# Kernel tuning notes

Hardware: AMD Instinct MI355X
Metric: run time of the kernel (lower is better)

Reference implementation:

```python
import jax, jax.numpy as jnp
import numpy as np

H = 4096
GROUP = 128          # per-token activation quant group, also weight block size
EPS = 1e-6
FP8_MAX = 448.0      # float8_e4m3fn max


def fp8_roundtrip(v):
    # simulate fp8 storage: cast to e4m3 and back to f32
    return v.astype(jnp.float8_e4m3fn).astype(jnp.float32)


def rms_norm(x, w):
    # vLLM RMSNorm: x * rsqrt(mean(x^2) + eps) * weight, computed in f32
    var = jnp.mean(x * x, axis=-1, keepdims=True)
    return x * jax.lax.rsqrt(var + EPS) * w


def fused_add_rms_norm(x, resid, w):
    z = x + resid
    return rms_norm(z, w), z


def group_quant_dequant(y):
    # dynamic per-token-group (1,128) symmetric fp8 quant, then dequant
    T, Hd = y.shape
    yg = y.reshape(T, Hd // GROUP, GROUP)
    amax = jnp.max(jnp.abs(yg), axis=-1, keepdims=True)
    scale = jnp.maximum(amax, 1e-12) / FP8_MAX
    q = fp8_roundtrip(yg / scale)
    return (q * scale).reshape(T, Hd)


def block_fp8_linear(y, wq, wscale):
    # W8A8 block fp8 GEMM: act quant (1,128) groups, weight (128,128) block scales.
    # Math-equivalent form: dequantize both operands, then GEMM.
    a = group_quant_dequant(y)                                   # [T, H]
    ws = jnp.repeat(jnp.repeat(wscale, GROUP, 0), GROUP, 1)       # [H, H]
    w = wq * ws                                                   # dequant weight
    return a @ w                                                  # [T, H]


def setup_inputs() -> dict:
    key = jax.random.key(0)
    ks = jax.random.split(key, 8)
    T = 16384
    x = jax.random.normal(ks[0], (T, H), dtype=jnp.float32)
    norm_w = jnp.ones((4, H), dtype=jnp.float32)
    # weights: rand in [0,1) stored as fp8 (simulated by roundtrip)
    w0 = fp8_roundtrip(jax.random.uniform(ks[1], (H, H), dtype=jnp.float32))
    w1 = fp8_roundtrip(jax.random.uniform(ks[2], (H, H), dtype=jnp.float32))
    w2 = fp8_roundtrip(jax.random.uniform(ks[3], (H, H), dtype=jnp.float32))
    sh = H // GROUP
    ws0 = jax.random.uniform(ks[4], (sh, sh), dtype=jnp.float32)
    ws1 = jax.random.uniform(ks[5], (sh, sh), dtype=jnp.float32)
    ws2 = jax.random.uniform(ks[6], (sh, sh), dtype=jnp.float32)
    return {"x": x, "norm_w": norm_w, "w0": w0, "w1": w1, "w2": w2,
            "ws0": ws0, "ws1": ws1, "ws2": ws2}


def reference(x, norm_w, w0, w1, w2, ws0, ws1, ws2):
    x = jax.nn.relu(x)
    resid = x
    y = rms_norm(x, norm_w[0])
    x2 = block_fp8_linear(y, w0, ws0)
    y2, resid = fused_add_rms_norm(x2, resid, norm_w[1])
    x3 = block_fp8_linear(y2, w1, ws1)
    y3, resid = fused_add_rms_norm(x3, resid, norm_w[2])
    x4 = block_fp8_linear(y3, w2, ws2)
    y4, resid = fused_add_rms_norm(x4, resid, norm_w[3])
    return y4
```

## Files before the change

kernel.cpp:

```cpp
#include <hip/hip_runtime.h>

typedef __attribute__((ext_vector_type(4))) float f32x4;
typedef __attribute__((ext_vector_type(4))) unsigned int u32x4;
typedef __attribute__((ext_vector_type(4))) int i32x4;
typedef __attribute__((ext_vector_type(8))) int i32x8;
typedef __attribute__((ext_vector_type(4))) unsigned short u16x4;
typedef unsigned char u8;
typedef unsigned short u16;
typedef unsigned int u32;

#define MBYTE (1024*1024)
#define TTOK 16384
#define HDIM 4096

__device__ __forceinline__ float f16tof32(u16 h) {
  _Float16 x;
  __builtin_memcpy(&x, &h, 2);
  return (float)x;
}
__device__ __forceinline__ u16 f32tof16(float f) {
  _Float16 x = (_Float16)f;
  u16 h;
  __builtin_memcpy(&h, &x, 2);
  return h;
}


__device__ __forceinline__ void gload_lds16(const void* g, void* l) {
  __builtin_amdgcn_global_load_lds((const __attribute__((address_space(1))) void*)g,
                                   (__attribute__((address_space(3))) void*)l, 16, 0, 0);
}

__global__ __launch_bounds__(256) void k_wconv(const float* __restrict__ w0,
                                               const float* __restrict__ w1,
                                               const float* __restrict__ w2,
                                               u8* __restrict__ out) {
  __shared__ float tl[64][68];
  const int tid = threadIdx.x;
  const int bn = blockIdx.x, bk = blockIdx.y, z = blockIdx.z;
  const float* W = (z == 0) ? w0 : (z == 1 ? w1 : w2);
  u8* o = out + (size_t)z * 16 * MBYTE;
#pragma unroll
  for (int it = 0; it < 4; ++it) {
    int idx = it * 256 + tid;
    int r = idx >> 4, c4 = idx & 15;
    f32x4 v = *(const f32x4*)(W + (size_t)(bk * 64 + r) * HDIM + bn * 64 + c4 * 4);
    *(f32x4*)&tl[r][c4 * 4] = v;
  }
  __syncthreads();
  {
    int n = tid >> 2, q4 = tid & 3;
    u32 dw[4];
#pragma unroll
    for (int d = 0; d < 4; ++d) {
      int k0 = (d >> 1) * 32 + q4 * 8 + (d & 1) * 4;
      int w = __builtin_amdgcn_cvt_pk_fp8_f32(tl[k0 + 0][n], tl[k0 + 1][n], 0, false);
      w = __builtin_amdgcn_cvt_pk_fp8_f32(tl[k0 + 2][n], tl[k0 + 3][n], w, true);
      dw[d] = (u32)w;
    }
    u32x4 pack = {dw[0], dw[1], dw[2], dw[3]};
    *(u32x4*)(o + (size_t)(bn * 64 + n) * HDIM + (bk >> 1) * 128 + (bk & 1) * 64 + q4 * 16) = pack;
  }
}

template <int MODE>
__global__ __launch_bounds__(256) void k_norm(const void* __restrict__ in_,
                                              u16* __restrict__ resid,
                                              const float* __restrict__ nw,
                                              u32* __restrict__ qout,
                                              float* __restrict__ asct,
                                              float* __restrict__ yout) {
  const int row = blockIdx.x, t = threadIdx.x;
  u16x4* residr = (u16x4*)(resid + (size_t)row * HDIM);
  f32x4 v[4];
  float ss = 0.f;
#pragma unroll
  for (int j = 0; j < 4; ++j) {
    f32x4 a;
    if (MODE == 1) {
      const u16x4* inr = (const u16x4*)((const u16*)in_ + (size_t)row * HDIM);
      u16x4 iv = inr[j * 256 + t];
      a.x = f16tof32(iv.x); a.y = f16tof32(iv.y);
      a.z = f16tof32(iv.z); a.w = f16tof32(iv.w);
    } else {
      const f32x4* inr = (const f32x4*)((const float*)in_ + (size_t)row * HDIM);
      a = inr[j * 256 + t];
    }
    if (MODE == 0) {
      a.x = fmaxf(a.x, 0.f); a.y = fmaxf(a.y, 0.f);
      a.z = fmaxf(a.z, 0.f); a.w = fmaxf(a.w, 0.f);
    } else {
      u16x4 rz = residr[j * 256 + t];
      a.x += f16tof32(rz.x); a.y += f16tof32(rz.y);
      a.z += f16tof32(rz.z); a.w += f16tof32(rz.w);
    }
    if (MODE < 2) {
      u16x4 rw;
      rw.x = f32tof16(a.x); rw.y = f32tof16(a.y);
      rw.z = f32tof16(a.z); rw.w = f32tof16(a.w);
      residr[j * 256 + t] = rw;
    }
    v[j] = a;
    ss += a.x * a.x + a.y * a.y + a.z * a.z + a.w * a.w;
  }
#pragma unroll
  for (int m = 1; m <= 32; m <<= 1) ss += __shfl_xor(ss, m, 64);
  __shared__ float sred[4];
  if ((t & 63) == 0) sred[t >> 6] = ss;
  __syncthreads();
  float tot = sred[0] + sred[1] + sred[2] + sred[3];
  float rinv = rsqrtf(tot * (1.f / (float)HDIM) + 1e-6f);
#pragma unroll
  for (int j = 0; j < 4; ++j) {
    f32x4 nv = ((const f32x4*)nw)[j * 256 + t];
    f32x4 y;
    y.x = v[j].x * rinv * nv.x; y.y = v[j].y * rinv * nv.y;
    y.z = v[j].z * rinv * nv.z; y.w = v[j].w * rinv * nv.w;
    if (MODE == 2) {
      ((f32x4*)yout)[(size_t)row * 1024 + j * 256 + t] = y;
    } else {
      float am = fmaxf(fmaxf(fabsf(y.x), fabsf(y.y)), fmaxf(fabsf(y.z), fabsf(y.w)));
#pragma unroll
      for (int m = 1; m <= 16; m <<= 1) am = fmaxf(am, __shfl_xor(am, m, 64));
      am = fmaxf(am, 1e-12f);
      float scale = am / 448.f;
      float inv = 448.f / am;
      int d = __builtin_amdgcn_cvt_pk_fp8_f32(y.x * inv, y.y * inv, 0, false);
      d = __builtin_amdgcn_cvt_pk_fp8_f32(y.z * inv, y.w * inv, d, true);
      int k4 = j * 256 + t;
      int k4w = k4 & 31;
      int k4n = (k4 & ~31) | (((k4w >> 4) & 1) << 4) | (((k4w >> 1) & 3) << 2)
              | (((k4w >> 3) & 1) << 1) | (k4w & 1);
      qout[(size_t)row * 1024 + k4n] = (u32)d;
      if ((t & 31) == 0) asct[(size_t)(j * 8 + (t >> 5)) * TTOK + row] = scale;
    }
  }
}

template <int F16OUT>
__global__ __launch_bounds__(256, 2) void k_gemm(const u8* __restrict__ A,
                                                 const u8* __restrict__ B,
                                                 const float* __restrict__ aS,
                                                 const float* __restrict__ bS,
                                                 void* __restrict__ C) {
  __shared__ u8 Al[2][128 * 128];
  __shared__ u8 Bl[2][128 * 128];
  __shared__ float As[32 * 128];
  const int tid = threadIdx.x;
  const int lane = tid & 63, wave = tid >> 6;
  const int lin = blockIdx.x;
  const int xcd = lin & 7, tt = lin >> 3;
  const int sidx = tt >> 3, rr = tt & 7;
  const int sm = sidx >> 3, sn = sidx & 7;
  const int bm = xcd * 16 + sm * 2 + (rr >> 2);
  const int bn = sn * 4 + (rr & 3);
  const int brow = bm * 128, bcol = bn * 128;
  const int wrb = (wave >> 1) * 64, wcb = (wave & 1) * 64;
  const int r16 = lane & 15, q4 = lane >> 4;
  const int swz3 = r16 & 7;
  const int c0 = (q4 ^ swz3) << 4;
  const int c1 = ((4 + q4) ^ swz3) << 4;

  const int srow = tid >> 3;
  const int scol = (((tid & 7) ^ (srow & 7)) << 4);
  const u8* aP = A + (size_t)(brow + srow) * HDIM + scol;
  const u8* bP = B + (size_t)(bcol + srow) * HDIM + scol;
  const int ldst = tid * 16;

#define STAGE(c, kt) do {                                                       \
    _Pragma("unroll")                                                           \
    for (int i = 0; i < 4; ++i) {                                               \
      gload_lds16(aP + (size_t)(kt) * 128 + (size_t)i * 32 * HDIM,              \
                  &Al[c][i * 4096 + ldst]);                                     \
      gload_lds16(bP + (size_t)(kt) * 128 + (size_t)i * 32 * HDIM,              \
                  &Bl[c][i * 4096 + ldst]);                                     \
    }                                                                           \
  } while (0)

  f32x4 av[4];
#pragma unroll
  for (int i = 0; i < 4; ++i) {
    const int kt_ = i * 8 + (tid >> 5);
    const int r_ = (tid & 31) * 4;
    av[i] = *(const f32x4*)(aS + (size_t)kt_ * TTOK + brow + r_);
  }
  STAGE(0, 0);
  STAGE(1, 1);
  asm volatile("s_waitcnt vmcnt(16)" ::: "memory");
#pragma unroll
  for (int i = 0; i < 4; ++i)
    *(f32x4*)&As[i * 1024 + tid * 4] = av[i];
  asm volatile("s_waitcnt lgkmcnt(0)" ::: "memory");

  f32x4 accm[4][4] = {};
  const f32x4 z4 = {0.f, 0.f, 0.f, 0.f};

#pragma unroll 1
  for (int kt = 0; kt < 32; ++kt) {
    const int cur = kt & 1;
    if (kt < 31) asm volatile("s_waitcnt vmcnt(8)" ::: "memory");
    else         asm volatile("s_waitcnt vmcnt(0)" ::: "memory");
    __builtin_amdgcn_s_barrier();
    __builtin_amdgcn_sched_barrier(0);

    const float wsb = bS[kt * 32 + bn];

    i32x8 bfr[4];
#pragma unroll
    for (int n = 0; n < 4; ++n) {
      const u8* rp = &Bl[cur][(wcb + n * 16 + r16) * 128];
      i32x4 lo = *(const i32x4*)(rp + c0);
      i32x4 hi = *(const i32x4*)(rp + c1);
      bfr[n] = __builtin_shufflevector(lo, hi, 0, 1, 2, 3, 4, 5, 6, 7);
    }

#pragma unroll
    for (int m = 0; m < 4; ++m) {
      const u8* rp = &Al[cur][(wrb + m * 16 + r16) * 128];
      i32x4 lo = *(const i32x4*)(rp + c0);
      i32x4 hi = *(const i32x4*)(rp + c1);
      i32x8 afr = __builtin_shufflevector(lo, hi, 0, 1, 2, 3, 4, 5, 6, 7);
      const f32x4 sa = *(const f32x4*)&As[kt * 128 + wrb + m * 16 + q4 * 4];
      const f32x4 s = sa * wsb;
      f32x4 acc[4];
      __builtin_amdgcn_s_setprio(1);
#pragma unroll
      for (int n = 0; n < 4; ++n)
        acc[n] = __builtin_amdgcn_mfma_scale_f32_16x16x128_f8f6f4(
            afr, bfr[n], z4, 0, 0, 0, 0x7F7F7F7F, 0, 0x7F7F7F7F);
      __builtin_amdgcn_s_setprio(0);
#pragma unroll
      for (int n = 0; n < 4; ++n)
        accm[m][n] += acc[n] * s;
    }

    __builtin_amdgcn_sched_barrier(0);
    __builtin_amdgcn_s_barrier();
    if (kt < 30) STAGE(cur, kt + 2);
  }
#undef STAGE

#pragma unroll
  for (int m = 0; m < 4; ++m) {
#pragma unroll
    for (int r = 0; r < 4; ++r) {
      const size_t rowi = (size_t)(brow + wrb + m * 16 + q4 * 4 + r);
      if (F16OUT) {
        u16* Cp = (u16*)C + rowi * HDIM + bcol + wcb + r16;
#pragma unroll
        for (int n = 0; n < 4; ++n) Cp[n * 16] = f32tof16(accm[m][n][r]);
      } else {
        float* Cp = (float*)C + rowi * HDIM + bcol + wcb + r16;
#pragma unroll
        for (int n = 0; n < 4; ++n) Cp[n * 16] = accm[m][n][r];
      }
    }
  }
}

extern "C" void kernel_launch(void* const* d_in, const int* in_sizes, int n_in,
                              void* d_out, int out_size, void* d_ws, size_t ws_size,
                              hipStream_t stream) {
  const float* x  = (const float*)d_in[0];
  const float* nw = (const float*)d_in[1];
  const float* w0 = (const float*)d_in[2];
  const float* w1 = (const float*)d_in[3];
  const float* w2 = (const float*)d_in[4];
  const float* s0 = (const float*)d_in[5];
  const float* s1 = (const float*)d_in[6];
  const float* s2 = (const float*)d_in[7];
  float* out = (float*)d_out;
  char* ws = (char*)d_ws;

  u8*  wqt   = (u8*)ws;
  u32* q     = (u32*)(ws + (size_t)48 * MBYTE);
  float* asc = (float*)(ws + (size_t)112 * MBYTE);
  u16* rsd   = (u16*)(ws + (size_t)114 * MBYTE);

  k_wconv<<<dim3(64, 64, 3), 256, 0, stream>>>(w0, w1, w2, wqt);

  k_norm<0><<<TTOK, 256, 0, stream>>>(x, rsd, nw, q, asc, nullptr);
  k_gemm<1><<<4096, 256, 0, stream>>>((const u8*)q, wqt, asc, s0, d_out);

  k_norm<1><<<TTOK, 256, 0, stream>>>(d_out, rsd, nw + HDIM, q, asc, nullptr);
  k_gemm<1><<<4096, 256, 0, stream>>>((const u8*)q, wqt + (size_t)16 * MBYTE, asc, s1, d_out);

  k_norm<1><<<TTOK, 256, 0, stream>>>(d_out, rsd, nw + 2 * HDIM, q, asc, nullptr);
  k_gemm<0><<<4096, 256, 0, stream>>>((const u8*)q, wqt + (size_t)32 * MBYTE, asc, s2, d_out);

  k_norm<2><<<TTOK, 256, 0, stream>>>(d_out, rsd, nw + 3 * HDIM, nullptr, nullptr, out);
}
```

Before: 1.387 ms.

## Fuse residual add into GEMM epilogue and ping-pong fp16 residual buffers

The residual addition moves from the norm kernel into the GEMM epilogue. The GEMM now reads the fp16 residual, adds it to the accumulator and writes the sum z as fp16. The norm kernels then only read z, with no separate residual read and write, and two ping-pong workspace buffers hold z between stages. The last GEMM also writes fp16 instead of f32, which cuts traffic but adds an extra rounding step before the final norm.

```diff
diff --git a/kernel.cpp b/kernel.cpp
--- a/kernel.cpp
+++ b/kernel.cpp
@@ -65,40 +65,31 @@
 
 template <int MODE>
 __global__ __launch_bounds__(256) void k_norm(const void* __restrict__ in_,
-                                              u16* __restrict__ resid,
+                                              u16* __restrict__ zout,
                                               const float* __restrict__ nw,
                                               u32* __restrict__ qout,
                                               float* __restrict__ asct,
                                               float* __restrict__ yout) {
   const int row = blockIdx.x, t = threadIdx.x;
-  u16x4* residr = (u16x4*)(resid + (size_t)row * HDIM);
   f32x4 v[4];
   float ss = 0.f;
 #pragma unroll
   for (int j = 0; j < 4; ++j) {
     f32x4 a;
-    if (MODE == 1) {
+    if (MODE == 0) {
+      const f32x4* inr = (const f32x4*)((const float*)in_ + (size_t)row * HDIM);
+      a = inr[j * 256 + t];
+      a.x = fmaxf(a.x, 0.f); a.y = fmaxf(a.y, 0.f);
+      a.z = fmaxf(a.z, 0.f); a.w = fmaxf(a.w, 0.f);
+      u16x4 rw;
+      rw.x = f32tof16(a.x); rw.y = f32tof16(a.y);
+      rw.z = f32tof16(a.z); rw.w = f32tof16(a.w);
+      ((u16x4*)(zout + (size_t)row * HDIM))[j * 256 + t] = rw;
+    } else {
       const u16x4* inr = (const u16x4*)((const u16*)in_ + (size_t)row * HDIM);
       u16x4 iv = inr[j * 256 + t];
       a.x = f16tof32(iv.x); a.y = f16tof32(iv.y);
       a.z = f16tof32(iv.z); a.w = f16tof32(iv.w);
-    } else {
-      const f32x4* inr = (const f32x4*)((const float*)in_ + (size_t)row * HDIM);
-      a = inr[j * 256 + t];
-    }
-    if (MODE == 0) {
-      a.x = fmaxf(a.x, 0.f); a.y = fmaxf(a.y, 0.f);
-      a.z = fmaxf(a.z, 0.f); a.w = fmaxf(a.w, 0.f);
-    } else {
-      u16x4 rz = residr[j * 256 + t];
-      a.x += f16tof32(rz.x); a.y += f16tof32(rz.y);
-      a.z += f16tof32(rz.z); a.w += f16tof32(rz.w);
-    }
-    if (MODE < 2) {
-      u16x4 rw;
-      rw.x = f32tof16(a.x); rw.y = f32tof16(a.y);
-      rw.z = f32tof16(a.z); rw.w = f32tof16(a.w);
-      residr[j * 256 + t] = rw;
     }
     v[j] = a;
     ss += a.x * a.x + a.y * a.y + a.z * a.z + a.w * a.w;
@@ -137,12 +128,12 @@
   }
 }
 
-template <int F16OUT>
 __global__ __launch_bounds__(256, 2) void k_gemm(const u8* __restrict__ A,
                                                  const u8* __restrict__ B,
                                                  const float* __restrict__ aS,
                                                  const float* __restrict__ bS,
-                                                 void* __restrict__ C) {
+                                                 const u16* __restrict__ resid,
+                                                 u16* __restrict__ Z) {
   __shared__ u8 Al[2][128 * 128];
   __shared__ u8 Bl[2][128 * 128];
   __shared__ float As[32 * 128];
@@ -245,15 +236,11 @@
 #pragma unroll
     for (int r = 0; r < 4; ++r) {
       const size_t rowi = (size_t)(brow + wrb + m * 16 + q4 * 4 + r);
-      if (F16OUT) {
-        u16* Cp = (u16*)C + rowi * HDIM + bcol + wcb + r16;
-#pragma unroll
-        for (int n = 0; n < 4; ++n) Cp[n * 16] = f32tof16(accm[m][n][r]);
-      } else {
-        float* Cp = (float*)C + rowi * HDIM + bcol + wcb + r16;
-#pragma unroll
-        for (int n = 0; n < 4; ++n) Cp[n * 16] = accm[m][n][r];
-      }
+      const u16* Rp = resid + rowi * HDIM + bcol + wcb + r16;
+      u16* Zp = Z + rowi * HDIM + bcol + wcb + r16;
+#pragma unroll
+      for (int n = 0; n < 4; ++n)
+        Zp[n * 16] = f32tof16(accm[m][n][r] + f16tof32(Rp[n * 16]));
     }
   }
 }
@@ -275,18 +262,19 @@
   u8*  wqt   = (u8*)ws;
   u32* q     = (u32*)(ws + (size_t)48 * MBYTE);
   float* asc = (float*)(ws + (size_t)112 * MBYTE);
-  u16* rsd   = (u16*)(ws + (size_t)114 * MBYTE);
+  u16* zA    = (u16*)(ws + (size_t)114 * MBYTE);
+  u16* zB    = (u16*)(ws + (size_t)242 * MBYTE);
 
   k_wconv<<<dim3(64, 64, 3), 256, 0, stream>>>(w0, w1, w2, wqt);
 
-  k_norm<0><<<TTOK, 256, 0, stream>>>(x, rsd, nw, q, asc, nullptr);
-  k_gemm<1><<<4096, 256, 0, stream>>>((const u8*)q, wqt, asc, s0, d_out);
-
-  k_norm<1><<<TTOK, 256, 0, stream>>>(d_out, rsd, nw + HDIM, q, asc, nullptr);
-  k_gemm<1><<<4096, 256, 0, stream>>>((const u8*)q, wqt + (size_t)16 * MBYTE, asc, s1, d_out);
-
-  k_norm<1><<<TTOK, 256, 0, stream>>>(d_out, rsd, nw + 2 * HDIM, q, asc, nullptr);
-  k_gemm<0><<<4096, 256, 0, stream>>>((const u8*)q, wqt + (size_t)32 * MBYTE, asc, s2, d_out);
-
-  k_norm<2><<<TTOK, 256, 0, stream>>>(d_out, rsd, nw + 3 * HDIM, nullptr, nullptr, out);
-}
+  k_norm<0><<<TTOK, 256, 0, stream>>>(x, zA, nw, q, asc, nullptr);
+  k_gemm<<<4096, 256, 0, stream>>>((const u8*)q, wqt, asc, s0, zA, zB);
+
+  k_norm<1><<<TTOK, 256, 0, stream>>>(zB, nullptr, nw + HDIM, q, asc, nullptr);
+  k_gemm<<<4096, 256, 0, stream>>>((const u8*)q, wqt + (size_t)16 * MBYTE, asc, s1, zB, zA);
+
+  k_norm<1><<<TTOK, 256, 0, stream>>>(zA, nullptr, nw + 2 * HDIM, q, asc, nullptr);
+  k_gemm<<<4096, 256, 0, stream>>>((const u8*)q, wqt + (size_t)32 * MBYTE, asc, s2, zA, zB);
+
+  k_norm<2><<<TTOK, 256, 0, stream>>>(zB, nullptr, nw + 3 * HDIM, nullptr, nullptr, out);
+}
```

Measured after the change: 1.296 ms. 1.07x faster.
